# Optimization experiments

Measured on AMD Instinct MI355X. Metric: run time of the kernel, lower is better.

The kernel has to match this reference:

```python
import jax, jax.numpy as jnp
import numpy as np

B, S, D, H, E, K = 2, 1024, 512, 2048, 8, 2

def setup_inputs() -> dict:
    key = jax.random.key(0)
    k1, k2, k3, k4, k5 = jax.random.split(key, 5)
    std = 0.02
    return {
        "x": jax.random.normal(k1, (B, S, D), dtype=jnp.float32),
        "indices": jax.random.randint(k2, (B, S, K), 0, E, dtype=jnp.int32),
        "weights": jax.random.uniform(k3, (B, S, K), dtype=jnp.float32),
        "keys": std * jax.random.normal(k4, (D, E, H), dtype=jnp.float32),
        "key_bias": jnp.zeros((E, H), dtype=jnp.float32),
        "values": std * jax.random.normal(k5, (H, E, D), dtype=jnp.float32),
        "value_bias": jnp.zeros((E, D), dtype=jnp.float32),
    }

def reference(x, indices, weights, keys, key_bias, values, value_bias):
    # Faithful to FeedForward.process_by_indices: for each token, run the FFN of
    # each of its top-k experts and sum results weighted by routing weights.
    # Expressed as dense all-expert compute + sparse one-hot combine (identical math).
    b, s, d = x.shape
    k = indices.shape[-1]
    e = keys.shape[1]
    xt = x.reshape(-1, d)                      # [T, D]
    idx = indices.reshape(-1, k)               # [T, K]
    w = weights.reshape(-1, k)                 # [T, K]
    # per-expert FFN for all tokens: hidden [T, E, H]
    hidden = jax.nn.gelu(jnp.einsum('td,deh->teh', xt, keys) + key_bias)
    out_e = jnp.einsum('teh,heo->teo', hidden, values) + value_bias  # [T, E, D]
    # combine matrix: sum_k weight_k * onehot(expert_k)  -> [T, E]
    comb = jnp.sum(jax.nn.one_hot(idx, e, dtype=xt.dtype) * w[..., None], axis=1)
    out = jnp.einsum('teo,te->to', out_e, comb)  # [T, D]
    return out.reshape(b, s, d)
```

## Files before the change

kernel.cpp:

```cpp
#include <hip/hip_runtime.h>
#include <hip/hip_bf16.h>

#define TB   2048
#define DD   512
#define HH   2048
#define EE   8
#define TK   4096

typedef __attribute__((ext_vector_type(8))) __bf16 bf16x8;
typedef __attribute__((ext_vector_type(4))) float  f32x4;

#define CONTRIB_ELEMS ((size_t)TK * DD)
#define KSPLIT1 2

__device__ __forceinline__ unsigned short f2bf(float f) {
  return __builtin_bit_cast(unsigned short, (__bf16)f);
}
__device__ __forceinline__ float bf2f(unsigned short h) {
  union { unsigned u; float f; } c; c.u = (unsigned)h << 16; return c.f;
}

__global__ void route_kernel(const int* __restrict__ idx, const float* __restrict__ wts,
                             int* cnt, int* offs, int* rowt, int* pos, float* wrow) {
  __shared__ int s_cnt[EE], s_off[EE], s_fill[EE];
  int tid = threadIdx.x;
  if (tid < EE) s_cnt[tid] = 0;
  __syncthreads();
  for (int i = tid; i < TK; i += 256) atomicAdd(&s_cnt[idx[i]], 1);
  __syncthreads();
  if (tid == 0) {
    int acc = 0;
    for (int e = 0; e < EE; ++e) { s_off[e] = acc; acc += s_cnt[e]; s_fill[e] = s_off[e]; }
  }
  __syncthreads();
  for (int i = tid; i < TK; i += 256) {
    int e = idx[i];
    int r = atomicAdd(&s_fill[e], 1);
    rowt[r] = i;
    pos[i]  = r;
    wrow[r] = wts[i];
  }
  if (tid < EE) { cnt[tid] = s_cnt[tid]; offs[tid] = s_off[tid]; }
}

__global__ __launch_bounds__(256) void prep_kernel(
    const float* __restrict__ x, const int* __restrict__ rowt, unsigned short* __restrict__ Xg,
    const float* __restrict__ keys, const float* __restrict__ values,
    unsigned short* __restrict__ kT, unsigned short* __restrict__ vT) {
  int bid = blockIdx.x;
  int tid = threadIdx.x;
  if (bid < 1024) {
    int i = bid * 256 + tid;
    int r = i >> 6;
    int c = i & 63;
    int t = rowt[r] >> 1;
    const float4* src = (const float4*)(x + (size_t)t * DD + c * 8);
    float4 a = src[0], b = src[1];
    unsigned short res[8];
    res[0]=f2bf(a.x); res[1]=f2bf(a.y); res[2]=f2bf(a.z); res[3]=f2bf(a.w);
    res[4]=f2bf(b.x); res[5]=f2bf(b.y); res[6]=f2bf(b.z); res[7]=f2bf(b.w);
    *(uint4*)(Xg + (size_t)r * DD + c * 8) = *(uint4*)res;
    return;
  }
  __shared__ unsigned short t[64][66];
  const float* src; unsigned short* dst;
  int e, k0, n0, SRCK, SRCE, KD, ND;
  if (bid < 3072) {
    int rel = bid - 1024; e = rel >> 8; int rem = rel & 255;
    k0 = (rem >> 5) * 64; n0 = (rem & 31) * 64;
    src = keys; dst = kT; SRCK = EE * HH; SRCE = HH; KD = DD; ND = HH;
  } else {
    int rel = bid - 3072; e = rel >> 8; int rem = rel & 255;
    k0 = (rem >> 3) * 64; n0 = (rem & 7) * 64;
    src = values; dst = vT; SRCK = EE * DD; SRCE = DD; KD = HH; ND = DD;
  }
  #pragma unroll
  for (int it = 0; it < 4; ++it) {
    int idx = tid + it * 256;
    int r  = idx >> 4;
    int c4 = idx & 15;
    float4 v = *(const float4*)(src + (size_t)(k0 + r) * SRCK + (size_t)e * SRCE + n0 + c4 * 4);
    unsigned short q[4] = {f2bf(v.x), f2bf(v.y), f2bf(v.z), f2bf(v.w)};
    *(uint2*)&t[r][c4 * 4] = *(uint2*)q;
  }
  __syncthreads();
  #pragma unroll
  for (int it = 0; it < 2; ++it) {
    int idx = tid + it * 256;
    int n  = idx >> 3;
    int kc = (idx & 7) * 8;
    unsigned short q[8];
    #pragma unroll
    for (int i = 0; i < 8; ++i) q[i] = t[kc + i][n];
    *(uint4*)(dst + ((size_t)e * ND + n0 + n) * KD + k0 + kc) = *(uint4*)q;
  }
}

template<int ROWS>
__device__ __forceinline__ void stage_swz(const char* src, int src_stride,
                                          unsigned short* lds, int wave, int lane) {
  constexpr int PW = ROWS * 128 / 1024 / 4;
  #pragma unroll
  for (int j = 0; j < PW; ++j) {
    int base = (wave * PW + j) * 1024;
    int o = base + lane * 16;
    int row  = o >> 7;
    int slot = (o >> 4) & 7;
    const char* g = src + (size_t)row * src_stride + ((slot ^ (row & 7)) << 4);
    __builtin_amdgcn_global_load_lds(
        (const __attribute__((address_space(1))) unsigned*)g,
        (__attribute__((address_space(3))) unsigned*)((char*)lds + base), 16, 0, 0);
  }
}

template<int BM, int BN, int PASS, int KSPLIT>
__device__ __forceinline__ void ffn_gemm_body(
    const unsigned short* __restrict__ Aall, const unsigned short* __restrict__ Bw,
    const float* __restrict__ bias,
    const int* __restrict__ cnt, const int* __restrict__ offs,
    const float* __restrict__ wrow,
    unsigned short* __restrict__ outA, unsigned short* __restrict__ outB)
{
  constexpr int KDIM = (PASS == 0) ? DD : HH;
  constexpr int NDIM = (PASS == 0) ? HH : DD;
  constexpr int KLEN = KDIM / KSPLIT;
  constexpr int NT   = KLEN / 64;
  constexpr int NX   = NDIM / BN;
  constexpr int NY   = TK / BM;
  constexpr int PER_E = NY * NX * KSPLIT;
  constexpr int NWG  = EE * PER_E;
  constexpr int WM = BM / 2, WN = BN / 2;
  constexpr int FM = WM / 16, FN = WN / 16;

  int bid = blockIdx.x;
  int swz = (bid & 7) * (NWG / 8) + (bid >> 3);
  int e   = swz / PER_E;
  int rem = swz % PER_E;
  int mblk = rem / (NX * KSPLIT);
  int r2   = rem % (NX * KSPLIT);
  int xblk = r2 / KSPLIT;
  int ks   = r2 % KSPLIT;

  const int n_e = cnt[e];
  if (mblk * BM >= n_e) return;
  const int off_e = offs[e];
  const int bn = xblk * BN;

  __shared__ __align__(1024) unsigned short Sb0[(BM + BN) * 64];
  __shared__ __align__(1024) unsigned short Sb1[(BM + BN) * 64];

  const int tid  = threadIdx.x;
  const int lane = tid & 63;
  const int wave = tid >> 6;
  const int wm = wave >> 1, wn = wave & 1;
  const int lr = lane & 15;
  const int kg = lane >> 4;

  const char* Ab = (const char*)(Aall + (size_t)(off_e + mblk * BM) * KDIM + ks * KLEN);
  const char* Bb = (const char*)(Bw + ((size_t)e * NDIM + bn) * KDIM + ks * KLEN);

  f32x4 acc[FM][FN] = {};

  auto STAGE = [&](unsigned short* buf, int kt) {
    stage_swz<BM>(Ab + kt * 128, KDIM * 2, buf, wave, lane);
    stage_swz<BN>(Bb + kt * 128, KDIM * 2, buf + BM * 64, wave, lane);
  };
  auto COMPUTE = [&](const unsigned short* buf) {
    const char* As = (const char*)buf;
    const char* Bs = (const char*)(buf + BM * 64);
    #pragma unroll
    for (int kss = 0; kss < 2; ++kss) {
      bf16x8 af[FM], bfv[FN];
      #pragma unroll
      for (int fm = 0; fm < FM; ++fm) {
        int r = wm * WM + fm * 16 + lr;
        int sl = (kss * 4 + kg) ^ (r & 7);
        af[fm] = *(const bf16x8*)(As + r * 128 + (sl << 4));
      }
      #pragma unroll
      for (int fn = 0; fn < FN; ++fn) {
        int r = wn * WN + fn * 16 + lr;
        int sl = (kss * 4 + kg) ^ (r & 7);
        bfv[fn] = *(const bf16x8*)(Bs + r * 128 + (sl << 4));
      }
      #pragma unroll
      for (int fm = 0; fm < FM; ++fm)
        #pragma unroll
        for (int fn = 0; fn < FN; ++fn)
          acc[fm][fn] = __builtin_amdgcn_mfma_f32_16x16x32_bf16(af[fm], bfv[fn], acc[fm][fn], 0, 0, 0);
    }
  };

  STAGE(Sb0, 0);
  __syncthreads();
  #pragma unroll 2
  for (int kt = 0; kt < NT; kt += 2) {
    if (kt + 1 < NT) STAGE(Sb1, kt + 1);
    COMPUTE(Sb0);
    __syncthreads();
    if (kt + 2 < NT) STAGE(Sb0, kt + 2);
    COMPUTE(Sb1);
    __syncthreads();
  }

  const int rq = kg * 4;
  #pragma unroll
  for (int fm = 0; fm < FM; ++fm) {
    int row0 = mblk * BM + wm * WM + fm * 16 + rq;
    #pragma unroll
    for (int fn = 0; fn < FN; ++fn) {
      int col = bn + wn * WN + fn * 16 + lr;
      float bs = (PASS == 0 || ks == 0) ? bias[e * NDIM + col] : 0.f;
      #pragma unroll
      for (int i = 0; i < 4; ++i) {
        int rl = row0 + i;
        if (rl < n_e) {
          float v = acc[fm][fn][i] + bs;
          if (PASS == 0) {
            float u = 0.7978845608f * (v + 0.044715f * v * v * v);
            float g = v / (1.f + __expf(-2.f * u));
            outA[(size_t)(off_e + rl) * HH + col] = f2bf(g);
          } else {
            float w = wrow[off_e + rl];
            outB[ks * CONTRIB_ELEMS + (size_t)(off_e + rl) * DD + col] = f2bf(v * w);
          }
        }
      }
    }
  }
}

__global__ __launch_bounds__(256, 5) void ffn_gemm_p0(
    const unsigned short* __restrict__ Aall, const unsigned short* __restrict__ Bw,
    const float* __restrict__ bias, const int* __restrict__ cnt, const int* __restrict__ offs,
    const float* __restrict__ wrow, unsigned short* __restrict__ outA) {
  ffn_gemm_body<64, 64, 0, 1>(Aall, Bw, bias, cnt, offs, wrow, outA, nullptr);
}
__global__ __launch_bounds__(256, 5) void ffn_gemm_p1(
    const unsigned short* __restrict__ Aall, const unsigned short* __restrict__ Bw,
    const float* __restrict__ bias, const int* __restrict__ cnt, const int* __restrict__ offs,
    const float* __restrict__ wrow, unsigned short* __restrict__ outB) {
  ffn_gemm_body<64, 64, 1, KSPLIT1>(Aall, Bw, bias, cnt, offs, wrow, nullptr, outB);
}

__global__ void combine(const unsigned short* __restrict__ contrib, const int* __restrict__ pos,
                        float* __restrict__ out) {
  int i = blockIdx.x * blockDim.x + threadIdx.x;
  int t = i >> 6;
  int c = i & 63;
  int r0 = pos[t * 2], r1 = pos[t * 2 + 1];
  float o[8] = {0,0,0,0,0,0,0,0};
  #pragma unroll
  for (int p = 0; p < KSPLIT1; ++p) {
    const unsigned short* base = contrib + (size_t)p * CONTRIB_ELEMS;
    union { uint4 q; unsigned short h[8]; } a, b;
    a.q = *(const uint4*)(base + (size_t)r0 * DD + c * 8);
    b.q = *(const uint4*)(base + (size_t)r1 * DD + c * 8);
    #pragma unroll
    for (int j = 0; j < 8; ++j)
      o[j] += bf2f(a.h[j]) + bf2f(b.h[j]);
  }
  float* dst = out + (size_t)t * DD + c * 8;
  *(float4*)dst       = *(float4*)&o[0];
  *(float4*)(dst + 4) = *(float4*)&o[4];
}

extern "C" void kernel_launch(void* const* d_in, const int* in_sizes, int n_in,
                              void* d_out, int out_size, void* d_ws, size_t ws_size,
                              hipStream_t stream) {
  const float* x          = (const float*)d_in[0];
  const int*   indices    = (const int*)d_in[1];
  const float* weights    = (const float*)d_in[2];
  const float* keys       = (const float*)d_in[3];
  const float* key_bias   = (const float*)d_in[4];
  const float* values     = (const float*)d_in[5];
  const float* value_bias = (const float*)d_in[6];
  float* out = (float*)d_out;

  char* ws = (char*)d_ws;
  int*   cnt  = (int*)(ws);
  int*   offs = (int*)(ws + 256);
  int*   rowt = (int*)(ws + 512);
  int*   pos  = (int*)(ws + 512 + 4 * TK);
  float* wrow = (float*)(ws + 512 + 8 * TK);
  unsigned short* Xg      = (unsigned short*)(ws + (64u << 10));
  unsigned short* hid     = (unsigned short*)(ws + (8u  << 20));
  unsigned short* kT      = (unsigned short*)(ws + (26u << 20));
  unsigned short* vT      = (unsigned short*)(ws + (43u << 20));
  unsigned short* contrib = (unsigned short*)(ws + (26u << 20));

  route_kernel<<<1, 256, 0, stream>>>(indices, weights, cnt, offs, rowt, pos, wrow);
  prep_kernel<<<5120, 256, 0, stream>>>(x, rowt, Xg, keys, values, kT, vT);

  ffn_gemm_p0<<<EE * (TK/64) * (HH/64), 256, 0, stream>>>(
      Xg, kT, key_bias, cnt, offs, wrow, hid);
  ffn_gemm_p1<<<EE * (TK/64) * (DD/64) * KSPLIT1, 256, 0, stream>>>(
      hid, vT, value_bias, cnt, offs, wrow, contrib);
  combine<<<(TB * 64) / 256, 256, 0, stream>>>(contrib, pos, out);
}
```

Measured before the change: 83.93 us.

## Replace combine pass with fp32 atomic scatter and overlap values transpose with pass 0

The second GEMM now adds its weighted outputs straight into the fp32 output through atomicAdd at the token's row. This removes the bf16 contrib buffer and the separate combine kernel, and the output is zeroed inside prep_kernel. The split-K factor for pass 1 goes from 2 to 4, and the values transpose moves out of prep into extra leading blocks of the pass-0 GEMM launch so it can overlap with that work. The cost is atomic contention on the output (eight adds per element across K-splits and the two experts) and a nondeterministic summation order.

```diff
diff --git a/kernel.cpp b/kernel.cpp
--- a/kernel.cpp
+++ b/kernel.cpp
@@ -9,15 +9,12 @@
 
 typedef __attribute__((ext_vector_type(8))) __bf16 bf16x8;
 typedef __attribute__((ext_vector_type(4))) float  f32x4;
-
-#define CONTRIB_ELEMS ((size_t)TK * DD)
-#define KSPLIT1 2
+typedef __attribute__((ext_vector_type(4))) unsigned int u32x4;
+
+#define KSPLIT1 4
 
 __device__ __forceinline__ unsigned short f2bf(float f) {
   return __builtin_bit_cast(unsigned short, (__bf16)f);
-}
-__device__ __forceinline__ float bf2f(unsigned short h) {
-  union { unsigned u; float f; } c; c.u = (unsigned)h << 16; return c.f;
 }
 
 __global__ void route_kernel(const int* __restrict__ idx, const float* __restrict__ wts,
@@ -45,11 +42,12 @@
 
 __global__ __launch_bounds__(256) void prep_kernel(
     const float* __restrict__ x, const int* __restrict__ rowt, unsigned short* __restrict__ Xg,
-    const float* __restrict__ keys, const float* __restrict__ values,
-    unsigned short* __restrict__ kT, unsigned short* __restrict__ vT) {
+    const float* __restrict__ keys, unsigned short* __restrict__ kT,
+    float* __restrict__ out) {
   int bid = blockIdx.x;
   int tid = threadIdx.x;
   if (bid < 1024) {
+    ((float4*)out)[bid * 256 + tid] = float4{0.f, 0.f, 0.f, 0.f};
     int i = bid * 256 + tid;
     int r = i >> 6;
     int c = i & 63;
@@ -62,26 +60,17 @@
     *(uint4*)(Xg + (size_t)r * DD + c * 8) = *(uint4*)res;
     return;
   }
-  __shared__ unsigned short t[64][66];
-  const float* src; unsigned short* dst;
-  int e, k0, n0, SRCK, SRCE, KD, ND;
-  if (bid < 3072) {
-    int rel = bid - 1024; e = rel >> 8; int rem = rel & 255;
-    k0 = (rem >> 5) * 64; n0 = (rem & 31) * 64;
-    src = keys; dst = kT; SRCK = EE * HH; SRCE = HH; KD = DD; ND = HH;
-  } else {
-    int rel = bid - 3072; e = rel >> 8; int rem = rel & 255;
-    k0 = (rem >> 3) * 64; n0 = (rem & 7) * 64;
-    src = values; dst = vT; SRCK = EE * DD; SRCE = DD; KD = HH; ND = DD;
-  }
+  __shared__ unsigned short tt[64][66];
+  int rel = bid - 1024; int e = rel >> 8; int rem = rel & 255;
+  int k0 = (rem >> 5) * 64, n0 = (rem & 31) * 64;
   #pragma unroll
   for (int it = 0; it < 4; ++it) {
     int idx = tid + it * 256;
     int r  = idx >> 4;
     int c4 = idx & 15;
-    float4 v = *(const float4*)(src + (size_t)(k0 + r) * SRCK + (size_t)e * SRCE + n0 + c4 * 4);
+    float4 v = *(const float4*)(keys + (size_t)(k0 + r) * (EE * HH) + (size_t)e * HH + n0 + c4 * 4);
     unsigned short q[4] = {f2bf(v.x), f2bf(v.y), f2bf(v.z), f2bf(v.w)};
-    *(uint2*)&t[r][c4 * 4] = *(uint2*)q;
+    *(uint2*)&tt[r][c4 * 4] = *(uint2*)q;
   }
   __syncthreads();
   #pragma unroll
@@ -91,8 +80,36 @@
     int kc = (idx & 7) * 8;
     unsigned short q[8];
     #pragma unroll
-    for (int i = 0; i < 8; ++i) q[i] = t[kc + i][n];
-    *(uint4*)(dst + ((size_t)e * ND + n0 + n) * KD + k0 + kc) = *(uint4*)q;
+    for (int i = 0; i < 8; ++i) q[i] = tt[kc + i][n];
+    *(uint4*)(kT + ((size_t)e * HH + n0 + n) * DD + k0 + kc) = *(uint4*)q;
+  }
+}
+
+__device__ __forceinline__ void vt_transpose(unsigned short* smem, const float* __restrict__ values,
+                                             unsigned short* __restrict__ vT, int bid, int tid) {
+  int e = bid & 7, rem = bid >> 3;
+  int k0 = (rem >> 3) * 64;
+  int n0 = (rem & 7) * 64;
+  unsigned short (*tt)[66] = (unsigned short(*)[66])smem;
+  #pragma unroll
+  for (int it = 0; it < 4; ++it) {
+    int idx = tid + it * 256;
+    int r = idx >> 4, c4 = idx & 15;
+    const f32x4* sp = (const f32x4*)(values + (size_t)(k0 + r) * (EE * DD) + (size_t)e * DD + n0 + c4 * 4);
+    f32x4 v = __builtin_nontemporal_load(sp);
+    unsigned short q[4] = {f2bf(v.x), f2bf(v.y), f2bf(v.z), f2bf(v.w)};
+    *(uint2*)&tt[r][c4 * 4] = *(uint2*)q;
+  }
+  __syncthreads();
+  #pragma unroll
+  for (int it = 0; it < 2; ++it) {
+    int idx = tid + it * 256;
+    int n = idx >> 3;
+    int kc = (idx & 7) * 8;
+    unsigned short q[8];
+    #pragma unroll
+    for (int i = 0; i < 8; ++i) q[i] = tt[kc + i][n];
+    __builtin_nontemporal_store(*(u32x4*)q, (u32x4*)(vT + ((size_t)e * DD + n0 + n) * HH + k0 + kc));
   }
 }
 
@@ -115,11 +132,12 @@
 
 template<int BM, int BN, int PASS, int KSPLIT>
 __device__ __forceinline__ void ffn_gemm_body(
+    int bid, unsigned short* smem,
     const unsigned short* __restrict__ Aall, const unsigned short* __restrict__ Bw,
     const float* __restrict__ bias,
     const int* __restrict__ cnt, const int* __restrict__ offs,
-    const float* __restrict__ wrow,
-    unsigned short* __restrict__ outA, unsigned short* __restrict__ outB)
+    const float* __restrict__ wrow, const int* __restrict__ rowt,
+    unsigned short* __restrict__ outA, float* __restrict__ fout)
 {
   constexpr int KDIM = (PASS == 0) ? DD : HH;
   constexpr int NDIM = (PASS == 0) ? HH : DD;
@@ -132,7 +150,6 @@
   constexpr int WM = BM / 2, WN = BN / 2;
   constexpr int FM = WM / 16, FN = WN / 16;
 
-  int bid = blockIdx.x;
   int swz = (bid & 7) * (NWG / 8) + (bid >> 3);
   int e   = swz / PER_E;
   int rem = swz % PER_E;
@@ -146,8 +163,8 @@
   const int off_e = offs[e];
   const int bn = xblk * BN;
 
-  __shared__ __align__(1024) unsigned short Sb0[(BM + BN) * 64];
-  __shared__ __align__(1024) unsigned short Sb1[(BM + BN) * 64];
+  unsigned short* Sb0 = smem;
+  unsigned short* Sb1 = smem + (BM + BN) * 64;
 
   const int tid  = threadIdx.x;
   const int lane = tid & 63;
@@ -222,7 +239,8 @@
             outA[(size_t)(off_e + rl) * HH + col] = f2bf(g);
           } else {
             float w = wrow[off_e + rl];
-            outB[ks * CONTRIB_ELEMS + (size_t)(off_e + rl) * DD + col] = f2bf(v * w);
+            int tkn = rowt[off_e + rl] >> 1;
+            atomicAdd(fout + (size_t)tkn * DD + col, v * w);
           }
         }
       }
@@ -233,36 +251,21 @@
 __global__ __launch_bounds__(256, 5) void ffn_gemm_p0(
     const unsigned short* __restrict__ Aall, const unsigned short* __restrict__ Bw,
     const float* __restrict__ bias, const int* __restrict__ cnt, const int* __restrict__ offs,
-    const float* __restrict__ wrow, unsigned short* __restrict__ outA) {
-  ffn_gemm_body<64, 64, 0, 1>(Aall, Bw, bias, cnt, offs, wrow, outA, nullptr);
+    const float* __restrict__ wrow, unsigned short* __restrict__ outA,
+    const float* __restrict__ values, unsigned short* __restrict__ vT) {
+  __shared__ __align__(1024) unsigned short smem[2 * (64 + 64) * 64];
+  int bid = blockIdx.x;
+  if (bid < 2048) { vt_transpose(smem, values, vT, bid, threadIdx.x); return; }
+  ffn_gemm_body<64, 64, 0, 1>(bid - 2048, smem, Aall, Bw, bias, cnt, offs, wrow,
+                              nullptr, outA, nullptr);
 }
 __global__ __launch_bounds__(256, 5) void ffn_gemm_p1(
     const unsigned short* __restrict__ Aall, const unsigned short* __restrict__ Bw,
     const float* __restrict__ bias, const int* __restrict__ cnt, const int* __restrict__ offs,
-    const float* __restrict__ wrow, unsigned short* __restrict__ outB) {
-  ffn_gemm_body<64, 64, 1, KSPLIT1>(Aall, Bw, bias, cnt, offs, wrow, nullptr, outB);
-}
-
-__global__ void combine(const unsigned short* __restrict__ contrib, const int* __restrict__ pos,
-                        float* __restrict__ out) {
-  int i = blockIdx.x * blockDim.x + threadIdx.x;
-  int t = i >> 6;
-  int c = i & 63;
-  int r0 = pos[t * 2], r1 = pos[t * 2 + 1];
-  float o[8] = {0,0,0,0,0,0,0,0};
-  #pragma unroll
-  for (int p = 0; p < KSPLIT1; ++p) {
-    const unsigned short* base = contrib + (size_t)p * CONTRIB_ELEMS;
-    union { uint4 q; unsigned short h[8]; } a, b;
-    a.q = *(const uint4*)(base + (size_t)r0 * DD + c * 8);
-    b.q = *(const uint4*)(base + (size_t)r1 * DD + c * 8);
-    #pragma unroll
-    for (int j = 0; j < 8; ++j)
-      o[j] += bf2f(a.h[j]) + bf2f(b.h[j]);
-  }
-  float* dst = out + (size_t)t * DD + c * 8;
-  *(float4*)dst       = *(float4*)&o[0];
-  *(float4*)(dst + 4) = *(float4*)&o[4];
+    const float* __restrict__ wrow, const int* __restrict__ rowt, float* __restrict__ fout) {
+  __shared__ __align__(1024) unsigned short smem[2 * (64 + 64) * 64];
+  ffn_gemm_body<64, 64, 1, KSPLIT1>(blockIdx.x, smem, Aall, Bw, bias, cnt, offs, wrow,
+                                    rowt, nullptr, fout);
 }
 
 extern "C" void kernel_launch(void* const* d_in, const int* in_sizes, int n_in,
@@ -287,14 +290,12 @@
   unsigned short* hid     = (unsigned short*)(ws + (8u  << 20));
   unsigned short* kT      = (unsigned short*)(ws + (26u << 20));
   unsigned short* vT      = (unsigned short*)(ws + (43u << 20));
-  unsigned short* contrib = (unsigned short*)(ws + (26u << 20));
 
   route_kernel<<<1, 256, 0, stream>>>(indices, weights, cnt, offs, rowt, pos, wrow);
-  prep_kernel<<<5120, 256, 0, stream>>>(x, rowt, Xg, keys, values, kT, vT);
-
-  ffn_gemm_p0<<<EE * (TK/64) * (HH/64), 256, 0, stream>>>(
-      Xg, kT, key_bias, cnt, offs, wrow, hid);
+  prep_kernel<<<3072, 256, 0, stream>>>(x, rowt, Xg, keys, kT, out);
+
+  ffn_gemm_p0<<<2048 + EE * (TK/64) * (HH/64), 256, 0, stream>>>(
+      Xg, kT, key_bias, cnt, offs, wrow, hid, values, vT);
   ffn_gemm_p1<<<EE * (TK/64) * (DD/64) * KSPLIT1, 256, 0, stream>>>(
-      hid, vT, value_bias, cnt, offs, wrow, contrib);
-  combine<<<(TB * 64) / 256, 256, 0, stream>>>(contrib, pos, out);
-}
+      hid, vT, value_bias, cnt, offs, wrow, rowt, out);
+}
```

Measured after the change: 102.1 us. +21.6%, slower.
